# Kernel optimization log

Measured on AMD Instinct MI355X. Metric: run time of the kernel, lower is better.

The kernel has to match this reference:

```python
import jax, jax.numpy as jnp
import numpy as np

H = 51  # hidden size hardcoded in the module
B, L = 2048, 999


def setup_inputs() -> dict:
    key = jax.random.key(0)
    ks = jax.random.split(key, 11)
    s = 0.1
    return {
        "x": jax.random.normal(ks[0], (B, L), dtype=jnp.float32),
        "W_ih1": jax.random.normal(ks[1], (4 * H, 1), dtype=jnp.float32) * s,
        "W_hh1": jax.random.normal(ks[2], (4 * H, H), dtype=jnp.float32) * s,
        "b_ih1": jax.random.normal(ks[3], (4 * H,), dtype=jnp.float32) * s,
        "b_hh1": jax.random.normal(ks[4], (4 * H,), dtype=jnp.float32) * s,
        "W_ih2": jax.random.normal(ks[5], (4 * H, H), dtype=jnp.float32) * s,
        "W_hh2": jax.random.normal(ks[6], (4 * H, H), dtype=jnp.float32) * s,
        "b_ih2": jax.random.normal(ks[7], (4 * H,), dtype=jnp.float32) * s,
        "b_hh2": jax.random.normal(ks[8], (4 * H,), dtype=jnp.float32) * s,
        "W_lin": jax.random.normal(ks[9], (1, H), dtype=jnp.float32) * s,
        "b_lin": jax.random.normal(ks[10], (1,), dtype=jnp.float32) * s,
    }


def _lstm_cell(xt, h, c, Wih, Whh, bih, bhh):
    # PyTorch LSTMCell: gates ordered (i, f, g, o)
    gates = xt @ Wih.T + bih + h @ Whh.T + bhh  # [B, 4H]
    i, f, g, o = jnp.split(gates, 4, axis=-1)
    c_new = jax.nn.sigmoid(f) * c + jax.nn.sigmoid(i) * jnp.tanh(g)
    h_new = jax.nn.sigmoid(o) * jnp.tanh(c_new)
    return h_new, c_new


def reference(x, W_ih1, W_hh1, b_ih1, b_hh1, W_ih2, W_hh2, b_ih2, b_hh2, W_lin, b_lin):
    b = x.shape[0]
    z = jnp.zeros((b, H), dtype=x.dtype)

    def step(carry, xt):
        h1, c1, h2, c2 = carry
        h1, c1 = _lstm_cell(xt[:, None], h1, c1, W_ih1, W_hh1, b_ih1, b_hh1)
        h2, c2 = _lstm_cell(h1, h2, c2, W_ih2, W_hh2, b_ih2, b_hh2)
        out = h2 @ W_lin.T + b_lin  # [B, 1]
        return (h1, c1, h2, c2), out[:, 0]

    xs = x.T  # [L, B] time-major for scan
    _, outs = jax.lax.scan(step, (z, z, z, z), xs)
    return outs.T  # [B, L]
```

## Files before the change

kernel.cpp:

```cpp
#include <hip/hip_runtime.h>
#include <math.h>

#define H 51
#define LSEQ 999
#define BTOT 2048
#define E 16
#define NBLK (BTOT / E)

#define ROWS 256
#define K1 64
#define K2 128

#define WS_W1 0
#define WS_W2 (WS_W1 + ROWS * K1)
#define WS_WL (WS_W2 + ROWS * K2)
#define WS_BL (WS_WL + 64)

#define FRAME 1024
#define NFRAMES 8
#define PART_OFF (NFRAMES * FRAME)
#define LDS_BYTES (PART_OFF + 2 * 128 * 4)

#define F_L1(b, s) ((b) * 2 + (s))
#define F_H2(b, s) (4 + (b) * 2 + (s))

typedef __attribute__((ext_vector_type(8))) short bf16x8;
typedef __attribute__((ext_vector_type(4))) float f32x4;

__global__ void prep_kernel(const float* __restrict__ Wih1, const float* __restrict__ Whh1,
                            const float* __restrict__ bih1, const float* __restrict__ bhh1,
                            const float* __restrict__ Wih2, const float* __restrict__ Whh2,
                            const float* __restrict__ bih2, const float* __restrict__ bhh2,
                            const float* __restrict__ Wlin, const float* __restrict__ blin,
                            float* __restrict__ ws) {
    int tid = threadIdx.x + blockIdx.x * blockDim.x;
    int nthr = blockDim.x * gridDim.x;
    for (int idx = tid; idx < ROWS * K1; idx += nthr) {
        int R = idx / K1, k = idx % K1;
        int u = R >> 2, m = R & 3;
        float v = 0.0f;
        if (u < H) {
            if (k < H) v = Whh1[(m * H + u) * H + k];
            else if (k == 62) v = bih1[m * H + u] + bhh1[m * H + u];
            else if (k == 63) v = Wih1[m * H + u];
        }
        ws[WS_W1 + idx] = v;
    }
    for (int idx = tid; idx < ROWS * K2; idx += nthr) {
        int R = idx / K2, k = idx % K2;
        int u = R >> 2, m = R & 3;
        float v = 0.0f;
        if (u < H) {
            if (k < H) v = Wih2[(m * H + u) * H + k];
            else if (k == 62) v = bih2[m * H + u] + bhh2[m * H + u];
            else if (k >= 64 && k < 64 + H) v = Whh2[(m * H + u) * H + (k - 64)];
        }
        ws[WS_W2 + idx] = v;
    }
    for (int u = tid; u < 64; u += nthr) ws[WS_WL + u] = (u < H) ? Wlin[u] : 0.0f;
    if (tid == 0) ws[WS_BL] = blin[0];
}

__device__ __forceinline__ short f2bf(float f) {
    unsigned u = __float_as_uint(f);
    unsigned r = (u + 0x7fffu + ((u >> 16) & 1u)) >> 16;
    return (short)r;
}
__device__ __forceinline__ float bf2f(short b) {
    return __uint_as_float(((unsigned)(unsigned short)b) << 16);
}
__device__ __forceinline__ float sigm(float x) {
    return __builtin_amdgcn_rcpf(1.0f + __expf(-x));
}
__device__ __forceinline__ float tanh_(float x) {
    return fmaf(-2.0f, __builtin_amdgcn_rcpf(__expf(2.0f * x) + 1.0f), 1.0f);
}
__device__ __forceinline__ void wr1(char* base, int f, int k, int e, short hi) {
    const int kk = k & 31;
    const int gg = (kk & 15) >> 2;
    const int j  = (kk & 3) + ((kk >> 4) << 2);
    const int off = (gg * 16 + e) * 16 + j * 2;
    *(short*)(base + (size_t)f * FRAME + off) = hi;
}
__device__ __forceinline__ bf16x8 ld_fr(const char* base, int f, int l) {
    return *(const bf16x8*)(base + (size_t)f * FRAME + (size_t)l * 16);
}

__global__ void __launch_bounds__(512, 1)
lstm_kernel(const float* __restrict__ x, const float* __restrict__ ws,
            float* __restrict__ out) {
    __shared__ __align__(16) char smem[LDS_BYTES];

    const int tid = threadIdx.x;
    const int w = tid >> 6;
    const int l = tid & 63;
    const int g = l >> 4;
    const int e = l & 15;

    for (int i = tid; i < LDS_BYTES / 4; i += 512) ((float*)smem)[i] = 0.0f;

    bf16x8 w1h[2][2], w1l[2][2], w2h[2][4], w2l[2][4];
    float wlr[2];
#pragma unroll
    for (int i = 0; i < 2; ++i) {
        const int T = w * 2 + i;
        const int rowA = T * 16 + e;
#pragma unroll
        for (int s = 0; s < 2; ++s) {
            bf16x8 hh, ll;
#pragma unroll
            for (int j = 0; j < 8; ++j) {
                const int k = s * 32 + ((j < 4) ? (4 * g + j) : (16 + 4 * g + (j - 4)));
                float wv = ws[WS_W1 + rowA * K1 + k];
                short hb = f2bf(wv);
                hh[j] = hb;
                ll[j] = f2bf(wv - bf2f(hb));
            }
            w1h[i][s] = hh; w1l[i][s] = ll;
        }
#pragma unroll
        for (int s = 0; s < 4; ++s) {
            bf16x8 hh, ll;
#pragma unroll
            for (int j = 0; j < 8; ++j) {
                const int k = s * 32 + ((j < 4) ? (4 * g + j) : (16 + 4 * g + (j - 4)));
                float wv = ws[WS_W2 + rowA * K2 + k];
                short hb = f2bf(wv);
                hh[j] = hb;
                ll[j] = f2bf(wv - bf2f(hb));
            }
            w2h[i][s] = hh; w2l[i][s] = ll;
        }
        wlr[i] = ws[WS_WL + T * 4 + g];
    }
    const float blv = ws[WS_BL];

    const int b0 = blockIdx.x * E;
    const float* xp = x + (size_t)(b0 + e) * LSEQ;
    float* pparts = (float*)(smem + PART_OFF);

    __syncthreads();

    if (tid < 32) {
        const int bb = tid >> 4, ee = tid & 15;
        *(short*)(smem + (size_t)F_L1(bb, 1) * FRAME + (48 + ee) * 16 + 12) = (short)0x3F80;
    }
    float xv = 0.0f;
    if (w == 0 && l < 16) {
        float x0 = xp[0];
        wr1(smem, F_L1(0, 1), 63, e, f2bf(x0));
        xv = xp[1];
    }

    float c1s[2] = {0.f, 0.f};
    float c2s[2] = {0.f, 0.f};

    __syncthreads();

    for (int t = 0; t <= LSEQ; ++t) {
        const int q = t & 1;

        bf16x8 a1f[2], h2f[2];
#pragma unroll
        for (int s = 0; s < 2; ++s) {
            a1f[s] = ld_fr(smem, F_L1(q, s), l);
            h2f[s] = ld_fr(smem, F_H2(q, s), l);
        }

        if (w == 1 && l < 16 && t >= 2) {
            const float* pp = pparts + (q ^ 1) * 128;
            float r = ((pp[l] + pp[16 + l]) + (pp[32 + l] + pp[48 + l])) +
                      ((pp[64 + l] + pp[80 + l]) + (pp[96 + l] + pp[112 + l]));
            out[(size_t)(b0 + l) * LSEQ + (t - 2)] = r + blv;
        }

        float xnew = 0.0f;
        if (w == 0 && l < 16) {
            xnew = xp[(t + 2 < LSEQ) ? (t + 2) : (LSEQ - 1)];
            wr1(smem, F_L1(q ^ 1, 1), 63, e, f2bf(xv));
        }

        f32x4 acc1[2], acc2a[2], acc2b[2];
#pragma unroll
        for (int i = 0; i < 2; ++i) {
            acc1[i]  = (f32x4){0.f, 0.f, 0.f, 0.f};
            acc2a[i] = (f32x4){0.f, 0.f, 0.f, 0.f};
            acc2b[i] = (f32x4){0.f, 0.f, 0.f, 0.f};
        }
        __builtin_amdgcn_s_setprio(1);
#pragma unroll
        for (int s = 0; s < 2; ++s)
#pragma unroll
            for (int i = 0; i < 2; ++i) {
                acc1[i]  = __builtin_amdgcn_mfma_f32_16x16x32_bf16(w1h[i][s],     a1f[s], acc1[i],  0, 0, 0);
                acc2a[i] = __builtin_amdgcn_mfma_f32_16x16x32_bf16(w2h[i][s],     a1f[s], acc2a[i], 0, 0, 0);
                acc2b[i] = __builtin_amdgcn_mfma_f32_16x16x32_bf16(w2h[i][s + 2], h2f[s], acc2b[i], 0, 0, 0);
                acc1[i]  = __builtin_amdgcn_mfma_f32_16x16x32_bf16(w1l[i][s],     a1f[s], acc1[i],  0, 0, 0);
                acc2a[i] = __builtin_amdgcn_mfma_f32_16x16x32_bf16(w2l[i][s],     a1f[s], acc2a[i], 0, 0, 0);
                acc2b[i] = __builtin_amdgcn_mfma_f32_16x16x32_bf16(w2l[i][s + 2], h2f[s], acc2b[i], 0, 0, 0);
            }
        __builtin_amdgcn_s_setprio(0);

#pragma unroll
        for (int i = 0; i < 2; ++i) {
            float ig = sigm(acc1[i][0]), fg = sigm(acc1[i][1]);
            float gg = tanh_(acc1[i][2]), og = sigm(acc1[i][3]);
            c1s[i] = fg * c1s[i] + ig * gg;
            float h1 = og * tanh_(c1s[i]);
            const int u = (w * 2 + i) * 4 + g;
            if (u < 62) wr1(smem, F_L1(q ^ 1, u >> 5), u, e, f2bf(h1));
        }

        if (t > 0) {
            float pr = 0.0f;
#pragma unroll
            for (int i = 0; i < 2; ++i) {
                f32x4 a2 = acc2a[i] + acc2b[i];
                float ig = sigm(a2[0]), fg = sigm(a2[1]);
                float gg = tanh_(a2[2]), og = sigm(a2[3]);
                c2s[i] = fg * c2s[i] + ig * gg;
                float h2 = og * tanh_(c2s[i]);
                const int u = (w * 2 + i) * 4 + g;
                wr1(smem, F_H2(q ^ 1, u >> 5), u, e, f2bf(h2));
                pr = fmaf(wlr[i], h2, pr);
            }
            pr += __shfl_xor(pr, 16);
            pr += __shfl_xor(pr, 32);
            if (l < 16) pparts[q * 128 + w * 16 + l] = pr;
        }

        __syncthreads();
        xv = xnew;
    }

    if (w == 1 && l < 16) {
        const float* pp = pparts + (LSEQ & 1) * 128;
        float r = ((pp[l] + pp[16 + l]) + (pp[32 + l] + pp[48 + l])) +
                  ((pp[64 + l] + pp[80 + l]) + (pp[96 + l] + pp[112 + l]));
        out[(size_t)(b0 + l) * LSEQ + (LSEQ - 1)] = r + blv;
    }
}

extern "C" void kernel_launch(void* const* d_in, const int* in_sizes, int n_in,
                              void* d_out, int out_size, void* d_ws, size_t ws_size,
                              hipStream_t stream) {
    const float* x    = (const float*)d_in[0];
    const float* Wih1 = (const float*)d_in[1];
    const float* Whh1 = (const float*)d_in[2];
    const float* bih1 = (const float*)d_in[3];
    const float* bhh1 = (const float*)d_in[4];
    const float* Wih2 = (const float*)d_in[5];
    const float* Whh2 = (const float*)d_in[6];
    const float* bih2 = (const float*)d_in[7];
    const float* bhh2 = (const float*)d_in[8];
    const float* Wlin = (const float*)d_in[9];
    const float* blin = (const float*)d_in[10];
    float* ws  = (float*)d_ws;
    float* out = (float*)d_out;

    hipLaunchKernelGGL(prep_kernel, dim3(64), dim3(256), 0, stream,
                       Wih1, Whh1, bih1, bhh1, Wih2, Whh2, bih2, bhh2, Wlin, blin, ws);
    hipLaunchKernelGGL(lstm_kernel, dim3(NBLK), dim3(512), 0, stream, x, ws, out);
}
```

Baseline: 1.003 ms.

## Split gate tiles across 16 waves instead of 8 per LSTM block

Doubles the block size from 512 to 1024 threads so each wave handles one 16-row gate tile instead of two. The per-step serial chain of MFMAs and gate activations per wave is halved, at the cost of a wider barrier each timestep and a 16-way partial sum for the linear output. Register pressure per thread drops because weight fragments are halved. There are still 128 blocks on the 256-CU device.

```diff
diff --git a/kernel.cpp b/kernel.cpp
--- a/kernel.cpp
+++ b/kernel.cpp
@@ -19,7 +19,7 @@
 #define FRAME 1024
 #define NFRAMES 8
 #define PART_OFF (NFRAMES * FRAME)
-#define LDS_BYTES (PART_OFF + 2 * 128 * 4)
+#define LDS_BYTES (PART_OFF + 2 * 256 * 4)
 
 #define F_L1(b, s) ((b) * 2 + (s))
 #define F_H2(b, s) (4 + (b) * 2 + (s))
@@ -86,7 +86,7 @@
     return *(const bf16x8*)(base + (size_t)f * FRAME + (size_t)l * 16);
 }
 
-__global__ void __launch_bounds__(512, 1)
+__global__ void __launch_bounds__(1024)
 lstm_kernel(const float* __restrict__ x, const float* __restrict__ ws,
             float* __restrict__ out) {
     __shared__ __align__(16) char smem[LDS_BYTES];
@@ -97,42 +97,37 @@
     const int g = l >> 4;
     const int e = l & 15;
 
-    for (int i = tid; i < LDS_BYTES / 4; i += 512) ((float*)smem)[i] = 0.0f;
-
-    bf16x8 w1h[2][2], w1l[2][2], w2h[2][4], w2l[2][4];
-    float wlr[2];
-#pragma unroll
-    for (int i = 0; i < 2; ++i) {
-        const int T = w * 2 + i;
-        const int rowA = T * 16 + e;
-#pragma unroll
-        for (int s = 0; s < 2; ++s) {
-            bf16x8 hh, ll;
-#pragma unroll
-            for (int j = 0; j < 8; ++j) {
-                const int k = s * 32 + ((j < 4) ? (4 * g + j) : (16 + 4 * g + (j - 4)));
-                float wv = ws[WS_W1 + rowA * K1 + k];
-                short hb = f2bf(wv);
-                hh[j] = hb;
-                ll[j] = f2bf(wv - bf2f(hb));
-            }
-            w1h[i][s] = hh; w1l[i][s] = ll;
-        }
-#pragma unroll
-        for (int s = 0; s < 4; ++s) {
-            bf16x8 hh, ll;
-#pragma unroll
-            for (int j = 0; j < 8; ++j) {
-                const int k = s * 32 + ((j < 4) ? (4 * g + j) : (16 + 4 * g + (j - 4)));
-                float wv = ws[WS_W2 + rowA * K2 + k];
-                short hb = f2bf(wv);
-                hh[j] = hb;
-                ll[j] = f2bf(wv - bf2f(hb));
-            }
-            w2h[i][s] = hh; w2l[i][s] = ll;
-        }
-        wlr[i] = ws[WS_WL + T * 4 + g];
-    }
+    for (int i = tid; i < LDS_BYTES / 4; i += 1024) ((float*)smem)[i] = 0.0f;
+
+    bf16x8 w1h[2], w1l[2], w2h[4], w2l[4];
+    const int rowA = w * 16 + e;
+#pragma unroll
+    for (int s = 0; s < 2; ++s) {
+        bf16x8 hh, ll;
+#pragma unroll
+        for (int j = 0; j < 8; ++j) {
+            const int k = s * 32 + ((j < 4) ? (4 * g + j) : (16 + 4 * g + (j - 4)));
+            float wv = ws[WS_W1 + rowA * K1 + k];
+            short hb = f2bf(wv);
+            hh[j] = hb;
+            ll[j] = f2bf(wv - bf2f(hb));
+        }
+        w1h[s] = hh; w1l[s] = ll;
+    }
+#pragma unroll
+    for (int s = 0; s < 4; ++s) {
+        bf16x8 hh, ll;
+#pragma unroll
+        for (int j = 0; j < 8; ++j) {
+            const int k = s * 32 + ((j < 4) ? (4 * g + j) : (16 + 4 * g + (j - 4)));
+            float wv = ws[WS_W2 + rowA * K2 + k];
+            short hb = f2bf(wv);
+            hh[j] = hb;
+            ll[j] = f2bf(wv - bf2f(hb));
+        }
+        w2h[s] = hh; w2l[s] = ll;
+    }
+    const float wlr = ws[WS_WL + w * 4 + g];
     const float blv = ws[WS_BL];
 
     const int b0 = blockIdx.x * E;
@@ -152,8 +147,7 @@
         xv = xp[1];
     }
 
-    float c1s[2] = {0.f, 0.f};
-    float c2s[2] = {0.f, 0.f};
+    float c1s = 0.f, c2s = 0.f;
 
     __syncthreads();
 
@@ -168,9 +162,12 @@
         }
 
         if (w == 1 && l < 16 && t >= 2) {
-            const float* pp = pparts + (q ^ 1) * 128;
-            float r = ((pp[l] + pp[16 + l]) + (pp[32 + l] + pp[48 + l])) +
-                      ((pp[64 + l] + pp[80 + l]) + (pp[96 + l] + pp[112 + l]));
+            const float* pp = pparts + (q ^ 1) * 256;
+            float r = 0.0f;
+#pragma unroll
+            for (int ww = 0; ww < 16; ww += 4)
+                r += ((pp[ww * 16 + l] + pp[(ww + 1) * 16 + l]) +
+                      (pp[(ww + 2) * 16 + l] + pp[(ww + 3) * 16 + l]));
             out[(size_t)(b0 + l) * LSEQ + (t - 2)] = r + blv;
         }
 
@@ -180,53 +177,42 @@
             wr1(smem, F_L1(q ^ 1, 1), 63, e, f2bf(xv));
         }
 
-        f32x4 acc1[2], acc2a[2], acc2b[2];
-#pragma unroll
-        for (int i = 0; i < 2; ++i) {
-            acc1[i]  = (f32x4){0.f, 0.f, 0.f, 0.f};
-            acc2a[i] = (f32x4){0.f, 0.f, 0.f, 0.f};
-            acc2b[i] = (f32x4){0.f, 0.f, 0.f, 0.f};
-        }
+        f32x4 acc1  = (f32x4){0.f, 0.f, 0.f, 0.f};
+        f32x4 acc2a = (f32x4){0.f, 0.f, 0.f, 0.f};
+        f32x4 acc2b = (f32x4){0.f, 0.f, 0.f, 0.f};
         __builtin_amdgcn_s_setprio(1);
 #pragma unroll
-        for (int s = 0; s < 2; ++s)
-#pragma unroll
-            for (int i = 0; i < 2; ++i) {
-                acc1[i]  = __builtin_amdgcn_mfma_f32_16x16x32_bf16(w1h[i][s],     a1f[s], acc1[i],  0, 0, 0);
-                acc2a[i] = __builtin_amdgcn_mfma_f32_16x16x32_bf16(w2h[i][s],     a1f[s], acc2a[i], 0, 0, 0);
-                acc2b[i] = __builtin_amdgcn_mfma_f32_16x16x32_bf16(w2h[i][s + 2], h2f[s], acc2b[i], 0, 0, 0);
-                acc1[i]  = __builtin_amdgcn_mfma_f32_16x16x32_bf16(w1l[i][s],     a1f[s], acc1[i],  0, 0, 0);
-                acc2a[i] = __builtin_amdgcn_mfma_f32_16x16x32_bf16(w2l[i][s],     a1f[s], acc2a[i], 0, 0, 0);
-                acc2b[i] = __builtin_amdgcn_mfma_f32_16x16x32_bf16(w2l[i][s + 2], h2f[s], acc2b[i], 0, 0, 0);
-            }
+        for (int s = 0; s < 2; ++s) {
+            acc1  = __builtin_amdgcn_mfma_f32_16x16x32_bf16(w1h[s],     a1f[s], acc1,  0, 0, 0);
+            acc2a = __builtin_amdgcn_mfma_f32_16x16x32_bf16(w2h[s],     a1f[s], acc2a, 0, 0, 0);
+            acc2b = __builtin_amdgcn_mfma_f32_16x16x32_bf16(w2h[s + 2], h2f[s], acc2b, 0, 0, 0);
+            acc1  = __builtin_amdgcn_mfma_f32_16x16x32_bf16(w1l[s],     a1f[s], acc1,  0, 0, 0);
+            acc2a = __builtin_amdgcn_mfma_f32_16x16x32_bf16(w2l[s],     a1f[s], acc2a, 0, 0, 0);
+            acc2b = __builtin_amdgcn_mfma_f32_16x16x32_bf16(w2l[s + 2], h2f[s], acc2b, 0, 0, 0);
+        }
         __builtin_amdgcn_s_setprio(0);
 
-#pragma unroll
-        for (int i = 0; i < 2; ++i) {
-            float ig = sigm(acc1[i][0]), fg = sigm(acc1[i][1]);
-            float gg = tanh_(acc1[i][2]), og = sigm(acc1[i][3]);
-            c1s[i] = fg * c1s[i] + ig * gg;
-            float h1 = og * tanh_(c1s[i]);
-            const int u = (w * 2 + i) * 4 + g;
+        {
+            float ig = sigm(acc1[0]), fg = sigm(acc1[1]);
+            float gg = tanh_(acc1[2]), og = sigm(acc1[3]);
+            c1s = fg * c1s + ig * gg;
+            float h1 = og * tanh_(c1s);
+            const int u = w * 4 + g;
             if (u < 62) wr1(smem, F_L1(q ^ 1, u >> 5), u, e, f2bf(h1));
         }
 
         if (t > 0) {
-            float pr = 0.0f;
-#pragma unroll
-            for (int i = 0; i < 2; ++i) {
-                f32x4 a2 = acc2a[i] + acc2b[i];
-                float ig = sigm(a2[0]), fg = sigm(a2[1]);
-                float gg = tanh_(a2[2]), og = sigm(a2[3]);
-                c2s[i] = fg * c2s[i] + ig * gg;
-                float h2 = og * tanh_(c2s[i]);
-                const int u = (w * 2 + i) * 4 + g;
-                wr1(smem, F_H2(q ^ 1, u >> 5), u, e, f2bf(h2));
-                pr = fmaf(wlr[i], h2, pr);
-            }
+            f32x4 a2 = acc2a + acc2b;
+            float ig = sigm(a2[0]), fg = sigm(a2[1]);
+            float gg = tanh_(a2[2]), og = sigm(a2[3]);
+            c2s = fg * c2s + ig * gg;
+            float h2 = og * tanh_(c2s);
+            const int u = w * 4 + g;
+            wr1(smem, F_H2(q ^ 1, u >> 5), u, e, f2bf(h2));
+            float pr = wlr * h2;
             pr += __shfl_xor(pr, 16);
             pr += __shfl_xor(pr, 32);
-            if (l < 16) pparts[q * 128 + w * 16 + l] = pr;
+            if (l < 16) pparts[q * 256 + w * 16 + l] = pr;
         }
 
         __syncthreads();
@@ -234,9 +220,12 @@
     }
 
     if (w == 1 && l < 16) {
-        const float* pp = pparts + (LSEQ & 1) * 128;
-        float r = ((pp[l] + pp[16 + l]) + (pp[32 + l] + pp[48 + l])) +
-                  ((pp[64 + l] + pp[80 + l]) + (pp[96 + l] + pp[112 + l]));
+        const float* pp = pparts + (LSEQ & 1) * 256;
+        float r = 0.0f;
+#pragma unroll
+        for (int ww = 0; ww < 16; ww += 4)
+            r += ((pp[ww * 16 + l] + pp[(ww + 1) * 16 + l]) +
+                  (pp[(ww + 2) * 16 + l] + pp[(ww + 3) * 16 + l]));
         out[(size_t)(b0 + l) * LSEQ + (LSEQ - 1)] = r + blv;
     }
 }
@@ -260,5 +249,5 @@
 
     hipLaunchKernelGGL(prep_kernel, dim3(64), dim3(256), 0, stream,
                        Wih1, Whh1, bih1, bhh1, Wih2, Whh2, bih2, bhh2, Wlin, blin, ws);
-    hipLaunchKernelGGL(lstm_kernel, dim3(NBLK), dim3(512), 0, stream, x, ws, out);
-}
+    hipLaunchKernelGGL(lstm_kernel, dim3(NBLK), dim3(1024), 0, stream, x, ws, out);
+}
```

Result: no change. 1.015 ms (+1.2%).
